# Performance work log

Hardware: AMD Instinct MI355X
Metric: run time of the kernel (lower is better)

## Reference

```python
import jax, jax.numpy as jnp
import numpy as np

LATENT_PACKET_SIZE = 16

def setup_inputs() -> dict:
    key = jax.random.key(0)
    z = jax.random.normal(key, (4096, 1, 8192), dtype=jnp.float32)
    return {"z": z}

def reference(z) -> jnp.ndarray:
    B = z.shape[0]
    D = z.shape[2]
    P = LATENT_PACKET_SIZE
    n_packets = D // P
    zp = z.reshape(B, n_packets, P)                      # (B, N, P)
    # sort packets within each sample by the first element of each packet
    inds = jnp.argsort(zp[:, :, 0], axis=1)              # (B, N) int
    z_ordered = jnp.take_along_axis(zp, inds[:, :, None], axis=1)  # batched gather
    return z_ordered.reshape(B, 1, n_packets * P)
```

## Files before the change

### kernel.cpp

```cpp
#include <hip/hip_runtime.h>


#define NPK 512
#define DIM 8192
#define NT  256

__global__ __launch_bounds__(NT, 4)
void sort_latent_kernel(const float* __restrict__ z, float* __restrict__ out) {
    __shared__ float4 row4[DIM / 4];
    __shared__ float  keys[NPK];
    __shared__ int    idxs[NPK];

    const int t = threadIdx.x;
    const size_t rowoff = (size_t)blockIdx.x * DIM;
    const float4* __restrict__ zin4 = (const float4*)(z + rowoff);
    float4* __restrict__ out4 = (float4*)(out + rowoff);

#pragma unroll
    for (int i = 0; i < DIM / 4 / NT; ++i)
        row4[t + NT * i] = zin4[t + NT * i];
    __syncthreads();

    const float* rowf = (const float*)row4;
    keys[t]      = rowf[t * 16];
    keys[t + NT] = rowf[(t + NT) * 16];
    idxs[t]      = t;
    idxs[t + NT] = t + NT;
    __syncthreads();

    for (int k = 2; k <= NPK; k <<= 1) {
        for (int j = k >> 1; j > 0; j >>= 1) {
            const int i = ((t & ~(j - 1)) << 1) | (t & (j - 1));
            const int p = i | j;
            const bool up = ((i & k) == 0);
            const float ka = keys[i], kb = keys[p];
            const int   ia = idxs[i], ib = idxs[p];
            const bool agtb = (ka > kb) || (ka == kb && ia > ib);
            if (agtb == up) {
                keys[i] = kb; keys[p] = ka;
                idxs[i] = ib; idxs[p] = ia;
            }
            __syncthreads();
        }
    }

#pragma unroll
    for (int i = 0; i < DIM / 4 / NT; ++i) {
        const int o = t + NT * i;
        const int src = idxs[o >> 2];
        out4[o] = row4[(src << 2) | (o & 3)];
    }
}

extern "C" void kernel_launch(void* const* d_in, const int* in_sizes, int n_in,
                              void* d_out, int out_size, void* d_ws, size_t ws_size,
                              hipStream_t stream) {
    const float* z = (const float*)d_in[0];
    float* out = (float*)d_out;
    const int nrows = in_sizes[0] / DIM;
    sort_latent_kernel<<<nrows, NT, 0, stream>>>(z, out);
}
```

Measured before the change: 232.9 us.

## Replace bitonic sort with per-wavefront rank counting and direct global gather

Each wavefront now handles one row, and a block holds four rows. Packet keys become order-preserving 64-bit integers with the packet index as a tiebreak, and each lane computes the ranks of its eight keys by comparing them against all 512 keys. This removes the many block-wide barriers of the bitonic network. The output is gathered straight from global memory through a permutation in shared memory, so the full row is no longer staged in LDS, which lowers LDS use and allows higher occupancy. The cost is O(N^2) comparisons per row and uncoalesced 16-byte global reads that rely on cache for reuse.

```diff
diff --git a/kernel.cpp b/kernel.cpp
--- a/kernel.cpp
+++ b/kernel.cpp
@@ -3,52 +3,54 @@
 
 #define NPK 512
 #define DIM 8192
+#define RPB 4
 #define NT  256
 
-__global__ __launch_bounds__(NT, 4)
+__global__ __launch_bounds__(NT, 8)
 void sort_latent_kernel(const float* __restrict__ z, float* __restrict__ out) {
-    __shared__ float4 row4[DIM / 4];
-    __shared__ float  keys[NPK];
-    __shared__ int    idxs[NPK];
+    __shared__ unsigned long long keys[RPB][NPK];
+    __shared__ unsigned short     srcp[RPB][NPK];
 
-    const int t = threadIdx.x;
-    const size_t rowoff = (size_t)blockIdx.x * DIM;
-    const float4* __restrict__ zin4 = (const float4*)(z + rowoff);
-    float4* __restrict__ out4 = (float4*)(out + rowoff);
+    const int lane = threadIdx.x & 63;
+    const int w    = threadIdx.x >> 6;
+    const int row  = blockIdx.x * RPB + w;
+    const float* __restrict__ rowin  = z   + (size_t)row * DIM;
+    float*       __restrict__ rowout = out + (size_t)row * DIM;
 
+    unsigned long long myk[8];
 #pragma unroll
-    for (int i = 0; i < DIM / 4 / NT; ++i)
-        row4[t + NT * i] = zin4[t + NT * i];
+    for (int i = 0; i < 8; ++i) {
+        const unsigned int p = (unsigned)(i * 64 + lane);
+        const unsigned int b = __float_as_uint(rowin[p * 16]);
+        const unsigned int u = b ^ (((unsigned)((int)b >> 31)) | 0x80000000u);
+        myk[i] = ((unsigned long long)u << 32) | p;
+        keys[w][p] = myk[i];
+    }
     __syncthreads();
 
-    const float* rowf = (const float*)row4;
-    keys[t]      = rowf[t * 16];
-    keys[t + NT] = rowf[(t + NT) * 16];
-    idxs[t]      = t;
-    idxs[t + NT] = t + NT;
+    unsigned int rank[8] = {0, 0, 0, 0, 0, 0, 0, 0};
+    const unsigned long long* __restrict__ kk = keys[w];
+    for (int j = 0; j < NPK; j += 2) {
+        const unsigned long long k0 = kk[j];
+        const unsigned long long k1 = kk[j + 1];
+#pragma unroll
+        for (int i = 0; i < 8; ++i) {
+            rank[i] += (unsigned)(k0 < myk[i]);
+            rank[i] += (unsigned)(k1 < myk[i]);
+        }
+    }
+#pragma unroll
+    for (int i = 0; i < 8; ++i)
+        srcp[w][rank[i]] = (unsigned short)(i * 64 + lane);
     __syncthreads();
 
-    for (int k = 2; k <= NPK; k <<= 1) {
-        for (int j = k >> 1; j > 0; j >>= 1) {
-            const int i = ((t & ~(j - 1)) << 1) | (t & (j - 1));
-            const int p = i | j;
-            const bool up = ((i & k) == 0);
-            const float ka = keys[i], kb = keys[p];
-            const int   ia = idxs[i], ib = idxs[p];
-            const bool agtb = (ka > kb) || (ka == kb && ia > ib);
-            if (agtb == up) {
-                keys[i] = kb; keys[p] = ka;
-                idxs[i] = ib; idxs[p] = ia;
-            }
-            __syncthreads();
-        }
-    }
-
-#pragma unroll
-    for (int i = 0; i < DIM / 4 / NT; ++i) {
-        const int o = t + NT * i;
-        const int src = idxs[o >> 2];
-        out4[o] = row4[(src << 2) | (o & 3)];
+    const float4* __restrict__ in4  = (const float4*)rowin;
+    float4*       __restrict__ out4 = (float4*)rowout;
+#pragma unroll 8
+    for (int i = 0; i < DIM / 4 / 64; ++i) {
+        const int o = i * 64 + lane;
+        const int s = (int)srcp[w][o >> 2];
+        out4[o] = in4[(s << 2) | (o & 3)];
     }
 }
 
@@ -58,5 +60,5 @@
     const float* z = (const float*)d_in[0];
     float* out = (float*)d_out;
     const int nrows = in_sizes[0] / DIM;
-    sort_latent_kernel<<<nrows, NT, 0, stream>>>(z, out);
+    sort_latent_kernel<<<nrows / RPB, NT, 0, stream>>>(z, out);
 }
```

Measured after the change: 251.9 us. +8.2%, slower.
